# Optimization experiments

Hardware: AMD Instinct MI355X
Metric: run time of the kernel (lower is better)

The kernel has to match this reference:

```python
import jax, jax.numpy as jnp
import numpy as np

B, N = 2, 8192
FUN, EMB = 7, 3
H = 512
HEADS = 8
DH = H // HEADS  # 64
G = 32           # slice_num
L = 4            # n_layers
OUT = 4
MLP_H = 4 * H


def _ln(x, g, b, eps=1e-5):
    m = x.mean(-1, keepdims=True)
    v = ((x - m) ** 2).mean(-1, keepdims=True)
    return (x - m) * jax.lax.rsqrt(v + eps) * g + b


def _forward(fun, emb, W_pre1, b_pre1, W_pre2, b_pre2, placeholder,
             ln1_g, ln1_b, Wfx, bfx, Wx, bx, Wslice, bslice, temp,
             Wq, Wk, Wv, Wo, bo, ln2_g, ln2_b, Wm1, bm1, Wm2, bm2,
             lnf_g, lnf_b, Wout, bout):
    b, n = fun.shape[0], fun.shape[1]
    gelu = lambda z: jax.nn.gelu(z, approximate=False)  # torch nn.GELU default (erf)
    # preprocess MLP (n_layers=0, res=False): act(pre(x)) -> post
    x = jnp.concatenate([emb, fun], axis=-1)            # [B,N,EMB+FUN]
    fx = gelu(x @ W_pre1 + b_pre1) @ W_pre2 + b_pre2    # [B,N,H]
    fx = fx + placeholder
    scale = DH ** -0.5
    for l in range(L):
        # --- physics attention (irregular mesh) ---
        h = _ln(fx, ln1_g[l], ln1_b[l])
        fx_mid = (h @ Wfx[l] + bfx[l]).reshape(b, n, HEADS, DH)  # bnhd
        x_mid = (h @ Wx[l] + bx[l]).reshape(b, n, HEADS, DH)
        logits = jnp.einsum('bnhd,dg->bnhg', x_mid, Wslice[l]) + bslice[l]
        sw = jax.nn.softmax(logits / temp[l][None, None, :, None], axis=-1)  # bnhg
        slice_mass = sw.sum(axis=1)                                   # bhg
        token = jnp.einsum('bnhd,bnhg->bhgd', fx_mid, sw)
        token = token / (slice_mass[..., None] + 1e-5)                # bhgd
        q = token @ Wq[l]
        k = token @ Wk[l]
        v = token @ Wv[l]
        attn = jax.nn.softmax(jnp.einsum('bhgd,bhkd->bhgk', q, k) * scale, axis=-1)
        out_tok = jnp.einsum('bhgk,bhkd->bhgd', attn, v)
        out = jnp.einsum('bhgd,bnhg->bnhd', out_tok, sw).reshape(b, n, H)
        fx = out @ Wo[l] + bo[l] + fx
        # --- LN + MLP (hidden = 4H) with residual ---
        h2 = _ln(fx, ln2_g[l], ln2_b[l])
        fx = gelu(h2 @ Wm1[l] + bm1[l]) @ Wm2[l] + bm2[l] + fx
    # last-layer head: LN -> Linear(out_dim)
    return _ln(fx, lnf_g, lnf_b) @ Wout + bout


def setup_inputs() -> dict:
    key = jax.random.key(0)
    ks = iter(jax.random.split(key, 64))
    nrm = lambda shape, s=0.02: jax.random.normal(next(ks), shape, jnp.float32) * s
    return dict(
        fun=jax.random.normal(next(ks), (B, N, FUN), jnp.float32),
        emb=jax.random.normal(next(ks), (B, N, EMB), jnp.float32),
        W_pre1=nrm((FUN + EMB, 2 * H)), b_pre1=jnp.zeros((2 * H,), jnp.float32),
        W_pre2=nrm((2 * H, H)), b_pre2=jnp.zeros((H,), jnp.float32),
        placeholder=nrm((H,), 1.0),
        ln1_g=jnp.ones((L, H), jnp.float32), ln1_b=jnp.zeros((L, H), jnp.float32),
        Wfx=nrm((L, H, H)), bfx=jnp.zeros((L, H), jnp.float32),
        Wx=nrm((L, H, H)), bx=jnp.zeros((L, H), jnp.float32),
        Wslice=nrm((L, DH, G), 0.1), bslice=jnp.zeros((L, G), jnp.float32),
        temp=jnp.full((L, HEADS), 0.5, jnp.float32),
        Wq=nrm((L, DH, DH)), Wk=nrm((L, DH, DH)), Wv=nrm((L, DH, DH)),
        Wo=nrm((L, H, H)), bo=jnp.zeros((L, H), jnp.float32),
        ln2_g=jnp.ones((L, H), jnp.float32), ln2_b=jnp.zeros((L, H), jnp.float32),
        Wm1=nrm((L, H, MLP_H)), bm1=jnp.zeros((L, MLP_H), jnp.float32),
        Wm2=nrm((L, MLP_H, H)), bm2=jnp.zeros((L, H), jnp.float32),
        lnf_g=jnp.ones((H,), jnp.float32), lnf_b=jnp.zeros((H,), jnp.float32),
        Wout=nrm((H, OUT)), bout=jnp.zeros((OUT,), jnp.float32),
    )


def reference(fun, emb, W_pre1, b_pre1, W_pre2, b_pre2, placeholder,
              ln1_g, ln1_b, Wfx, bfx, Wx, bx, Wslice, bslice, temp,
              Wq, Wk, Wv, Wo, bo, ln2_g, ln2_b, Wm1, bm1, Wm2, bm2,
              lnf_g, lnf_b, Wout, bout):
    return _forward(fun, emb, W_pre1, b_pre1, W_pre2, b_pre2, placeholder,
                    ln1_g, ln1_b, Wfx, bfx, Wx, bx, Wslice, bslice, temp,
                    Wq, Wk, Wv, Wo, bo, ln2_g, ln2_b, Wm1, bm1, Wm2, bm2,
                    lnf_g, lnf_b, Wout, bout)
```

## Files before the change

### kernel.cpp

```cpp
#include <hip/hip_runtime.h>
#include <hip/hip_bf16.h>
#include <cstdint>
#include <cstddef>

typedef float  f32x4  __attribute__((ext_vector_type(4)));
typedef __bf16 bf16x8 __attribute__((ext_vector_type(8)));

#define DEV __device__ __forceinline__

DEV float gelu_f(float x){ return 0.5f * x * (1.0f + erff(x * 0.70710678118654752f)); }

DEV void gl16(void* lds, const void* g){
  __builtin_amdgcn_global_load_lds((const __attribute__((address_space(1))) void*)g,
                                   (__attribute__((address_space(3))) void*)lds, 16, 0, 0);
}

static constexpr size_t OFF_FX     = 0;
static constexpr size_t OFF_H      = 33554432;
static constexpr size_t OFF_REGA   = 50331648;
static constexpr size_t OFF_COMB   = OFF_REGA;
static constexpr size_t OFF_SW     = OFF_REGA + 50331648;
static constexpr size_t OFF_MLPH   = OFF_REGA;
static constexpr size_t OFF_H1     = OFF_REGA;
static constexpr size_t OFF_OUTB   = OFF_REGA + 67108864;
static constexpr size_t OFF_PT     = OFF_OUTB + 16777216;
static constexpr size_t OFF_PTM    = OFF_PT + 2097152;
static constexpr size_t OFF_OT     = OFF_PTM + 32768;
static constexpr size_t OFF_WT     = OFF_OT + 131072;
static constexpr size_t OFF_BIAS   = OFF_WT + 23068672;

__global__ __launch_bounds__(256) void wtrans_k(const float* __restrict__ W, __bf16* __restrict__ Wt,
                                                int K, int N, size_t wstride, size_t wtstride)
{
  __shared__ float tile[64][65];
  W  += (size_t)blockIdx.z * wstride;
  Wt += (size_t)blockIdx.z * wtstride;
  int t = threadIdx.x;
  int k0 = blockIdx.x * 64, n0 = blockIdx.y * 64;
  #pragma unroll
  for (int i = 0; i < 16; i++){
    int e = t + 256*i; int kk = e >> 6, nn = e & 63;
    tile[kk][nn] = W[(size_t)(k0+kk)*N + n0+nn];
  }
  __syncthreads();
  #pragma unroll
  for (int i = 0; i < 16; i++){
    int e = t + 256*i; int nn = e >> 6, kk = e & 63;
    Wt[(size_t)(n0+nn)*K + k0+kk] = (__bf16)tile[kk][nn];
  }
}

__global__ __launch_bounds__(128) void prep_wxs_k(const float* __restrict__ Wx, const float* __restrict__ Wsl,
                                                  const float* __restrict__ bx, const float* __restrict__ bsl,
                                                  const float* __restrict__ temp,
                                                  __bf16* __restrict__ Btcat, float* __restrict__ bcat)
{
  __shared__ float wsc[64];
  int l = blockIdx.y;
  const float* Wx_l  = Wx  + (size_t)l*262144;
  const float* Wsl_l = Wsl + l*2048;
  const float* bx_l  = bx  + l*512;
  const float* bsl_l = bsl + l*32;
  __bf16* Wt_l = Btcat + (size_t)l*393216 + (size_t)512*512;
  float* blog_l = bcat + l*768 + 512;
  int hg = blockIdx.x; int h = hg >> 5, g = hg & 31;
  int t = threadIdx.x;
  if (t < 64) wsc[t] = Wsl_l[t*32 + g];
  __syncthreads();
  float invt = 1.0f / temp[l*8 + h];
  #pragma unroll
  for (int cc = 0; cc < 4; cc++){
    int c = t + cc*128;
    float a = 0.f;
    for (int d = 0; d < 64; d++) a += Wx_l[(size_t)c*512 + h*64 + d] * wsc[d];
    Wt_l[(size_t)hg*512 + c] = (__bf16)(a * invt);
  }
  if (t == 0){
    float a = 0.f;
    for (int d = 0; d < 64; d++) a += bx_l[h*64 + d] * wsc[d];
    blog_l[hg] = (a + bsl_l[g]) * invt;
  }
}

__global__ __launch_bounds__(256) void bias_setup_k(const float* __restrict__ b_pre2, const float* __restrict__ placeholder,
                                                    const float* __restrict__ bfx,
                                                    float* __restrict__ bpre2p, float* __restrict__ bcat)
{
  int i = blockIdx.x*256 + threadIdx.x;
  if (i < 512) bpre2p[i] = b_pre2[i] + placeholder[i];
  else if (i < 2560){
    int j = i - 512; int l = j >> 9, c = j & 511;
    bcat[l*768 + c] = bfx[l*512 + c];
  }
}

__global__ __launch_bounds__(256) void preproc1_k(const float* __restrict__ fun, const float* __restrict__ emb,
                                                  const float* __restrict__ W1, const float* __restrict__ b1,
                                                  __bf16* __restrict__ h1)
{
  __shared__ float w1l[10][1024];
  int t = threadIdx.x;
  for (int i = t*4; i < 10240; i += 1024) *(f32x4*)&w1l[0][i] = *(const f32x4*)&W1[i];
  __syncthreads();
  f32x4 bv = *(const f32x4*)&b1[t*4];
  int r0 = blockIdx.x * 4;
  for (int r = 0; r < 4; r++){
    int m = r0 + r;
    const float* er = emb + (size_t)m*3;
    const float* fr = fun + (size_t)m*7;
    float x[10];
    x[0]=er[0]; x[1]=er[1]; x[2]=er[2];
    #pragma unroll
    for (int c = 0; c < 7; c++) x[3+c] = fr[c];
    f32x4 acc = bv;
    #pragma unroll
    for (int c = 0; c < 10; c++){
      f32x4 wv = *(const f32x4*)&w1l[c][t*4];
      acc += x[c] * wv;
    }
    __bf16* op = h1 + (size_t)m*1024 + t*4;
    #pragma unroll
    for (int e = 0; e < 4; e++) op[e] = (__bf16)gelu_f(acc[e]);
  }
}

template<int EPI, int BN>
__global__ __launch_bounds__(512) void gemm_wide(const __bf16* __restrict__ A, const __bf16* __restrict__ Bt,
                                                 const float* __restrict__ bias, const float* __restrict__ res,
                                                 void* __restrict__ outp, int N, int lgK)
{
  constexpr int NSUB_B = BN/16;
  constexpr int S = 16 + NSUB_B;
  constexpr int Q = S/8;
  constexpr int NJ = BN/32;
  __shared__ bf16x8 ldsAB[3][S][64];
  const int tid = threadIdx.x;
  const int w = tid >> 6, lane = tid & 63;
  const int lm = lane & 15, lq = lane >> 4;
  const int wr = w >> 1, wc = w & 1;
  const int m0 = blockIdx.x * 256, n0 = blockIdx.y * BN;
  const int niter = 1 << (lgK - 5);

  auto issue = [&](int i){
    unsigned buf = (unsigned)i % 3u;
    int kk = i << 5;
    #pragma unroll
    for (int q = 0; q < Q; q++){
      int f = w*Q + q;
      const __bf16* p = (f < 16)
        ? A  + (((size_t)(m0 + f*16 + lm)) << lgK) + kk + lq*8
        : Bt + (((size_t)(n0 + (f-16)*16 + lm)) << lgK) + kk + lq*8;
      gl16(&ldsAB[buf][f][0], p);
    }
  };

  issue(0); issue(1);

  f32x4 acc[4][NJ] = {};

  for (int i = 0; i < niter; ++i){
    if (i + 2 < niter){
      issue(i + 2);
      if constexpr (Q == 4) __builtin_amdgcn_s_waitcnt(0x0F78);
      else                  __builtin_amdgcn_s_waitcnt(0x0F76);
    } else if (i + 1 < niter){
      if constexpr (Q == 4) __builtin_amdgcn_s_waitcnt(0x0F74);
      else                  __builtin_amdgcn_s_waitcnt(0x0F73);
    } else {
      __builtin_amdgcn_s_waitcnt(0x0F70);
    }
    __builtin_amdgcn_s_barrier();
    const unsigned buf = (unsigned)i % 3u;
    bf16x8 af[4], bfr[NJ];
    #pragma unroll
    for (int ii = 0; ii < 4; ii++)  af[ii]  = ldsAB[buf][wr*4 + ii][lane];
    #pragma unroll
    for (int jj = 0; jj < NJ; jj++) bfr[jj] = ldsAB[buf][16 + wc*NJ + jj][lane];
    #pragma unroll
    for (int ii = 0; ii < 4; ii++)
      #pragma unroll
      for (int jj = 0; jj < NJ; jj++)
        acc[ii][jj] = __builtin_amdgcn_mfma_f32_16x16x32_bf16(af[ii], bfr[jj], acc[ii][jj], 0, 0, 0);
    __builtin_amdgcn_s_barrier();
  }

  #pragma unroll
  for (int ii = 0; ii < 4; ii++){
    int row0 = m0 + wr*64 + ii*16 + lq*4;
    #pragma unroll
    for (int jj = 0; jj < NJ; jj++){
      int col = n0 + wc*(BN/2) + jj*16 + lm;
      float bv = bias[col];
      #pragma unroll
      for (int r = 0; r < 4; r++){
        size_t idx = (size_t)(row0 + r)*N + col;
        float v = acc[ii][jj][r] + bv;
        if (EPI == 2) v += res[idx];
        if (EPI == 1) ((__bf16*)outp)[idx] = (__bf16)gelu_f(v);
        else          ((float*)outp)[idx]  = v;
      }
    }
  }
}

__global__ __launch_bounds__(256) void ln_k(const float* __restrict__ x, const float* __restrict__ g,
                                            const float* __restrict__ b, __bf16* __restrict__ out)
{
  int w = threadIdx.x >> 6, lane = threadIdx.x & 63;
  int row = blockIdx.x*4 + w;
  const float* xr = x + (size_t)row*512 + lane*8;
  float v[8];
  *(f32x4*)&v[0] = *(const f32x4*)xr;
  *(f32x4*)&v[4] = *(const f32x4*)(xr + 4);
  float s = 0.f, sq = 0.f;
  #pragma unroll
  for (int e = 0; e < 8; e++){ s += v[e]; sq += v[e]*v[e]; }
  #pragma unroll
  for (int off = 32; off; off >>= 1){ s += __shfl_xor(s, off); sq += __shfl_xor(sq, off); }
  float mean = s * (1.f/512.f);
  float var  = sq * (1.f/512.f) - mean*mean;
  float rstd = rsqrtf(var + 1e-5f);
  float gv[8], bv[8];
  *(f32x4*)&gv[0] = *(const f32x4*)(g + lane*8);
  *(f32x4*)&gv[4] = *(const f32x4*)(g + lane*8 + 4);
  *(f32x4*)&bv[0] = *(const f32x4*)(b + lane*8);
  *(f32x4*)&bv[4] = *(const f32x4*)(b + lane*8 + 4);
  __bf16* op = out + (size_t)row*512 + lane*8;
  #pragma unroll
  for (int e = 0; e < 8; e++) op[e] = (__bf16)((v[e]-mean)*rstd*gv[e] + bv[e]);
}

__global__ __launch_bounds__(256) void softmax_k(const float* __restrict__ comb, float* __restrict__ sw)
{
  int gid = blockIdx.x*256 + threadIdx.x;
  int m = gid >> 3, h = gid & 7;
  const float* lp = comb + (size_t)m*768 + 512 + h*32;
  float x[32];
  #pragma unroll
  for (int i = 0; i < 8; i++) *(f32x4*)&x[i*4] = *(const f32x4*)(lp + i*4);
  float mx = x[0];
  #pragma unroll
  for (int i = 1; i < 32; i++) mx = fmaxf(mx, x[i]);
  float s = 0.f;
  #pragma unroll
  for (int i = 0; i < 32; i++){ x[i] = expf(x[i]-mx); s += x[i]; }
  float inv = 1.f / s;
  int b = m >> 13, n = m & 8191;
  float* op = sw + ((size_t)(b*8 + h)*8192 + n)*32;
  #pragma unroll
  for (int i = 0; i < 8; i++){
    f32x4 t = *(f32x4*)&x[i*4];
    t *= inv;
    *(f32x4*)(op + i*4) = t;
  }
}

__global__ __launch_bounds__(256) void token_part_k(const float* __restrict__ comb, const float* __restrict__ sw,
                                                    float* __restrict__ pt, float* __restrict__ ptm)
{
  __shared__ float fxl[32][64];
  __shared__ float swl[32][32];
  int t = threadIdx.x;
  int chunk = blockIdx.x, bh = blockIdx.y;
  int b = bh >> 3, h = bh & 7;
  int d = t & 63, gg = (t >> 6) * 8;
  float acc[8] = {0,0,0,0,0,0,0,0};
  float macc = 0.f;
  for (int s = 0; s < 16; s++){
    int nbase = chunk*512 + s*32;
    __syncthreads();
    #pragma unroll
    for (int i = 0; i < 2; i++){
      int e = t + 256*i; int rv = e >> 4, c4 = e & 15;
      *(f32x4*)&fxl[rv][c4*4] = *(const f32x4*)&comb[((size_t)b*8192 + nbase + rv)*768 + h*64 + c4*4];
    }
    { int rv = t >> 3, c4 = t & 7;
      *(f32x4*)&swl[rv][c4*4] = *(const f32x4*)&sw[((size_t)bh*8192 + nbase + rv)*32 + c4*4]; }
    __syncthreads();
    for (int nn = 0; nn < 32; nn++){
      float f = fxl[nn][d];
      #pragma unroll
      for (int jj = 0; jj < 8; jj++) acc[jj] += f * swl[nn][gg+jj];
    }
    if (t < 32){ for (int nn = 0; nn < 32; nn++) macc += swl[nn][t]; }
  }
  int cb = chunk*16 + bh;
  #pragma unroll
  for (int jj = 0; jj < 8; jj++)
    pt[((size_t)cb*32 + gg + jj)*64 + d] = acc[jj];
  if (t < 32) ptm[cb*32 + t] = macc;
}

__global__ __launch_bounds__(256) void attn_k(const float* __restrict__ pt, const float* __restrict__ ptm,
                                              const float* __restrict__ Wq, const float* __restrict__ Wk,
                                              const float* __restrict__ Wv, float* __restrict__ ot)
{
  __shared__ float tok[32][64];
  __shared__ float ml[32];
  __shared__ float qq[32][65], kk2[32][65], vv[32][65];
  __shared__ float at[32][33];
  int t = threadIdx.x, bh = blockIdx.x;
  if (t < 32){
    float s = 0.f;
    for (int c = 0; c < 16; c++) s += ptm[(c*16 + bh)*32 + t];
    ml[t] = s + 1e-5f;
  }
  __syncthreads();
  #pragma unroll
  for (int i = 0; i < 8; i++){
    int e = t + 256*i; int g = e >> 6, d = e & 63;
    float s = 0.f;
    for (int c = 0; c < 16; c++) s += pt[((size_t)(c*16 + bh)*32 + g)*64 + d];
    tok[g][d] = s / ml[g];
  }
  __syncthreads();
  #pragma unroll
  for (int i = 0; i < 8; i++){
    int e = t + 256*i; int g = e >> 6, j = e & 63;
    float aq = 0.f, ak = 0.f, av = 0.f;
    for (int d = 0; d < 64; d++){
      float tv = tok[g][d];
      aq += tv * Wq[d*64 + j];
      ak += tv * Wk[d*64 + j];
      av += tv * Wv[d*64 + j];
    }
    qq[g][j] = aq; kk2[g][j] = ak; vv[g][j] = av;
  }
  __syncthreads();
  #pragma unroll
  for (int i = 0; i < 4; i++){
    int e = t + 256*i; int g = e >> 5, j2 = e & 31;
    float s2 = 0.f;
    for (int d = 0; d < 64; d++) s2 += qq[g][d] * kk2[j2][d];
    at[g][j2] = s2 * 0.125f;
  }
  __syncthreads();
  if (t < 32){
    float mx = at[t][0];
    for (int j = 1; j < 32; j++) mx = fmaxf(mx, at[t][j]);
    float ss = 0.f;
    for (int j = 0; j < 32; j++){ float e2 = expf(at[t][j]-mx); at[t][j] = e2; ss += e2; }
    float inv = 1.f / ss;
    for (int j = 0; j < 32; j++) at[t][j] *= inv;
  }
  __syncthreads();
  #pragma unroll
  for (int i = 0; i < 8; i++){
    int e = t + 256*i; int g = e >> 6, d = e & 63;
    float s3 = 0.f;
    for (int j = 0; j < 32; j++) s3 += at[g][j] * vv[j][d];
    ot[(size_t)bh*2048 + e] = s3;
  }
}

__global__ __launch_bounds__(256) void deslice_k(const float* __restrict__ ot, const float* __restrict__ sw,
                                                 __bf16* __restrict__ outb)
{
  __shared__ float otl[32][64];
  __shared__ float swl[4][33];
  int t = threadIdx.x;
  int chunk = blockIdx.x, bh = blockIdx.y;
  int b = bh >> 3, h = bh & 7;
  #pragma unroll
  for (int i = 0; i < 8; i++){
    int e = t + 256*i;
    otl[e>>6][e&63] = ot[(size_t)bh*2048 + e];
  }
  int n0 = chunk*128;
  int nsub = t >> 6, d = t & 63;
  for (int s = 0; s < 32; s++){
    __syncthreads();
    if (t < 128) swl[t>>5][t&31] = sw[((size_t)bh*8192 + n0 + s*4 + (t>>5))*32 + (t&31)];
    __syncthreads();
    float a2 = 0.f;
    #pragma unroll
    for (int g = 0; g < 32; g++) a2 += otl[g][d] * swl[nsub][g];
    int n = n0 + s*4 + nsub;
    outb[((size_t)(b*8192 + n))*512 + h*64 + d] = (__bf16)a2;
  }
}

__global__ __launch_bounds__(256) void head_k(const float* __restrict__ x, const float* __restrict__ g,
                                              const float* __restrict__ b, const float* __restrict__ Wout,
                                              const float* __restrict__ bout, float* __restrict__ out)
{
  int w = threadIdx.x >> 6, lane = threadIdx.x & 63;
  int row = blockIdx.x*4 + w;
  const float* xr = x + (size_t)row*512 + lane*8;
  float v[8];
  *(f32x4*)&v[0] = *(const f32x4*)xr;
  *(f32x4*)&v[4] = *(const f32x4*)(xr + 4);
  float s = 0.f, sq = 0.f;
  #pragma unroll
  for (int e = 0; e < 8; e++){ s += v[e]; sq += v[e]*v[e]; }
  #pragma unroll
  for (int off = 32; off; off >>= 1){ s += __shfl_xor(s, off); sq += __shfl_xor(sq, off); }
  float mean = s * (1.f/512.f);
  float rstd = rsqrtf(sq * (1.f/512.f) - mean*mean + 1e-5f);
  float o[4] = {0,0,0,0};
  #pragma unroll
  for (int e = 0; e < 8; e++){
    int c = lane*8 + e;
    float yn = (v[e]-mean)*rstd*g[c] + b[c];
    const float* wr = Wout + (size_t)c*4;
    o[0] += yn*wr[0]; o[1] += yn*wr[1]; o[2] += yn*wr[2]; o[3] += yn*wr[3];
  }
  #pragma unroll
  for (int off = 32; off; off >>= 1){
    #pragma unroll
    for (int j = 0; j < 4; j++) o[j] += __shfl_xor(o[j], off);
  }
  if (lane == 0){
    #pragma unroll
    for (int j = 0; j < 4; j++) out[(size_t)row*4 + j] = o[j] + bout[j];
  }
}

extern "C" void kernel_launch(void* const* d_in, const int* in_sizes, int n_in,
                              void* d_out, int out_size, void* d_ws, size_t ws_size,
                              hipStream_t stream)
{
  const float* fun    = (const float*)d_in[0];
  const float* emb    = (const float*)d_in[1];
  const float* W_pre1 = (const float*)d_in[2];
  const float* b_pre1 = (const float*)d_in[3];
  const float* W_pre2 = (const float*)d_in[4];
  const float* b_pre2 = (const float*)d_in[5];
  const float* placeholder = (const float*)d_in[6];
  const float* ln1_g  = (const float*)d_in[7];
  const float* ln1_b  = (const float*)d_in[8];
  const float* Wfx    = (const float*)d_in[9];
  const float* bfx    = (const float*)d_in[10];
  const float* Wx     = (const float*)d_in[11];
  const float* bx     = (const float*)d_in[12];
  const float* Wslice = (const float*)d_in[13];
  const float* bslice = (const float*)d_in[14];
  const float* temp   = (const float*)d_in[15];
  const float* Wq     = (const float*)d_in[16];
  const float* Wk     = (const float*)d_in[17];
  const float* Wv     = (const float*)d_in[18];
  const float* Wo     = (const float*)d_in[19];
  const float* bo     = (const float*)d_in[20];
  const float* ln2_g  = (const float*)d_in[21];
  const float* ln2_b  = (const float*)d_in[22];
  const float* Wm1    = (const float*)d_in[23];
  const float* bm1    = (const float*)d_in[24];
  const float* Wm2    = (const float*)d_in[25];
  const float* bm2    = (const float*)d_in[26];
  const float* lnf_g  = (const float*)d_in[27];
  const float* lnf_b  = (const float*)d_in[28];
  const float* Wout   = (const float*)d_in[29];
  const float* bout   = (const float*)d_in[30];

  char* ws = (char*)d_ws;
  float*  fx     = (float*)(ws + OFF_FX);
  __bf16* hbf    = (__bf16*)(ws + OFF_H);
  float*  comb   = (float*)(ws + OFF_COMB);
  float*  sw     = (float*)(ws + OFF_SW);
  __bf16* mlph   = (__bf16*)(ws + OFF_MLPH);
  __bf16* h1bf   = (__bf16*)(ws + OFF_H1);
  __bf16* outb   = (__bf16*)(ws + OFF_OUTB);
  float*  pt     = (float*)(ws + OFF_PT);
  float*  ptm    = (float*)(ws + OFF_PTM);
  float*  ot     = (float*)(ws + OFF_OT);
  __bf16* Wpre2t = (__bf16*)(ws + OFF_WT);
  __bf16* Btcat  = (__bf16*)(ws + OFF_WT + 1048576);
  __bf16* Wot    = (__bf16*)(ws + OFF_WT + 4194304);
  __bf16* Wm1t   = (__bf16*)(ws + OFF_WT + 6291456);
  __bf16* Wm2t   = (__bf16*)(ws + OFF_WT + 14680064);
  float*  bcat   = (float*)(ws + OFF_BIAS);
  float*  bpre2p = (float*)(ws + OFF_BIAS + 4*768*4);

  wtrans_k<<<dim3(16,8,1), 256,0,stream>>>(W_pre2, Wpre2t, 1024, 512, 0, 0);
  wtrans_k<<<dim3(8,8,4),  256,0,stream>>>(Wfx, Btcat, 512, 512, 262144, 393216);
  wtrans_k<<<dim3(8,8,4),  256,0,stream>>>(Wo,  Wot,  512, 512, 262144, 262144);
  wtrans_k<<<dim3(8,32,4), 256,0,stream>>>(Wm1, Wm1t, 512, 2048, 1048576, 1048576);
  wtrans_k<<<dim3(32,8,4), 256,0,stream>>>(Wm2, Wm2t, 2048, 512, 1048576, 1048576);
  prep_wxs_k<<<dim3(256,4),128,0,stream>>>(Wx, Wslice, bx, bslice, temp, Btcat, bcat);
  bias_setup_k<<<10,256,0,stream>>>(b_pre2, placeholder, bfx, bpre2p, bcat);

  preproc1_k<<<4096,256,0,stream>>>(fun, emb, W_pre1, b_pre1, h1bf);
  gemm_wide<0,128><<<dim3(64,4),512,0,stream>>>(h1bf, Wpre2t, bpre2p, nullptr, (void*)fx, 512, 10);

  for (int l = 0; l < 4; l++){
    ln_k<<<4096,256,0,stream>>>(fx, ln1_g + l*512, ln1_b + l*512, hbf);
    gemm_wide<0,256><<<dim3(64,3),512,0,stream>>>(hbf, Btcat + (size_t)l*393216, bcat + l*768, nullptr, (void*)comb, 768, 9);
    softmax_k<<<512,256,0,stream>>>(comb, sw);
    token_part_k<<<dim3(16,16),256,0,stream>>>(comb, sw, pt, ptm);
    attn_k<<<16,256,0,stream>>>(pt, ptm, Wq + l*4096, Wk + l*4096, Wv + l*4096, ot);
    deslice_k<<<dim3(64,16),256,0,stream>>>(ot, sw, outb);
    gemm_wide<2,128><<<dim3(64,4),512,0,stream>>>(outb, Wot + (size_t)l*262144, bo + l*512, fx, (void*)fx, 512, 9);
    ln_k<<<4096,256,0,stream>>>(fx, ln2_g + l*512, ln2_b + l*512, hbf);
    gemm_wide<1,256><<<dim3(64,8),512,0,stream>>>(hbf, Wm1t + (size_t)l*1048576, bm1 + l*2048, nullptr, (void*)mlph, 2048, 9);
    gemm_wide<2,128><<<dim3(64,4),512,0,stream>>>(mlph, Wm2t + (size_t)l*1048576, bm2 + l*512, fx, (void*)fx, 512, 11);
  }

  head_k<<<4096,256,0,stream>>>(fx, lnf_g, lnf_b, Wout, bout, (float*)d_out);
}
```

Before: 1.439 ms.

## Fuse slice softmax into projection GEMM epilogue and use double-buffered LDS

The per-head slice softmax moves into the epilogue of the combined fx/x/slice-logit GEMM. Blocks covering the logit columns compute the softmax with 16-lane shuffles and write slice weights directly, so the separate softmax kernel and its reread of the logits are gone. The GEMM pipeline also drops from triple to double LDS buffering with a prefetch distance of one. That reduces shared memory use, which may raise occupancy, but exposes more global-load latency. The epilogue writes are scalar strided stores rather than vectorized ones.

```diff
diff --git a/kernel.cpp b/kernel.cpp
--- a/kernel.cpp
+++ b/kernel.cpp
@@ -127,13 +127,14 @@
 template<int EPI, int BN>
 __global__ __launch_bounds__(512) void gemm_wide(const __bf16* __restrict__ A, const __bf16* __restrict__ Bt,
                                                  const float* __restrict__ bias, const float* __restrict__ res,
-                                                 void* __restrict__ outp, int N, int lgK)
+                                                 void* __restrict__ outp, void* __restrict__ outp2,
+                                                 int N, int lgK)
 {
   constexpr int NSUB_B = BN/16;
   constexpr int S = 16 + NSUB_B;
   constexpr int Q = S/8;
   constexpr int NJ = BN/32;
-  __shared__ bf16x8 ldsAB[3][S][64];
+  __shared__ bf16x8 ldsAB[2][S][64];
   const int tid = threadIdx.x;
   const int w = tid >> 6, lane = tid & 63;
   const int lm = lane & 15, lq = lane >> 4;
@@ -142,7 +143,7 @@
   const int niter = 1 << (lgK - 5);
 
   auto issue = [&](int i){
-    unsigned buf = (unsigned)i % 3u;
+    unsigned buf = (unsigned)i & 1u;
     int kk = i << 5;
     #pragma unroll
     for (int q = 0; q < Q; q++){
@@ -154,23 +155,20 @@
     }
   };
 
-  issue(0); issue(1);
+  issue(0);
 
   f32x4 acc[4][NJ] = {};
 
   for (int i = 0; i < niter; ++i){
-    if (i + 2 < niter){
-      issue(i + 2);
-      if constexpr (Q == 4) __builtin_amdgcn_s_waitcnt(0x0F78);
-      else                  __builtin_amdgcn_s_waitcnt(0x0F76);
-    } else if (i + 1 < niter){
+    if (i + 1 < niter){
+      issue(i + 1);
       if constexpr (Q == 4) __builtin_amdgcn_s_waitcnt(0x0F74);
       else                  __builtin_amdgcn_s_waitcnt(0x0F73);
     } else {
       __builtin_amdgcn_s_waitcnt(0x0F70);
     }
     __builtin_amdgcn_s_barrier();
-    const unsigned buf = (unsigned)i % 3u;
+    const unsigned buf = (unsigned)i & 1u;
     bf16x8 af[4], bfr[NJ];
     #pragma unroll
     for (int ii = 0; ii < 4; ii++)  af[ii]  = ldsAB[buf][wr*4 + ii][lane];
@@ -182,6 +180,40 @@
       for (int jj = 0; jj < NJ; jj++)
         acc[ii][jj] = __builtin_amdgcn_mfma_f32_16x16x32_bf16(af[ii], bfr[jj], acc[ii][jj], 0, 0, 0);
     __builtin_amdgcn_s_barrier();
+  }
+
+  if (EPI == 4 && blockIdx.y == 2){
+    float* swp = (float*)outp2;
+    #pragma unroll
+    for (int ii = 0; ii < 4; ii++){
+      int row0 = m0 + wr*64 + ii*16 + lq*4;
+      #pragma unroll
+      for (int hp = 0; hp < 4; hp++){
+        int j0 = hp*2, j1 = j0 + 1;
+        int h = wc*4 + hp;
+        float b0 = bias[512 + wc*128 + j0*16 + lm];
+        float b1 = bias[512 + wc*128 + j1*16 + lm];
+        #pragma unroll
+        for (int r = 0; r < 4; r++){
+          int row = row0 + r;
+          float v0 = acc[ii][j0][r] + b0;
+          float v1 = acc[ii][j1][r] + b1;
+          float mx = fmaxf(v0, v1);
+          #pragma unroll
+          for (int msk = 8; msk; msk >>= 1) mx = fmaxf(mx, __shfl_xor(mx, msk));
+          float e0 = expf(v0 - mx), e1 = expf(v1 - mx);
+          float ss = e0 + e1;
+          #pragma unroll
+          for (int msk = 8; msk; msk >>= 1) ss += __shfl_xor(ss, msk);
+          float inv = 1.f / ss;
+          int b = row >> 13, n = row & 8191;
+          float* op = swp + ((size_t)(b*8 + h)*8192 + n)*32;
+          op[lm]      = e0 * inv;
+          op[16 + lm] = e1 * inv;
+        }
+      }
+    }
+    return;
   }
 
   #pragma unroll
@@ -228,31 +260,6 @@
   __bf16* op = out + (size_t)row*512 + lane*8;
   #pragma unroll
   for (int e = 0; e < 8; e++) op[e] = (__bf16)((v[e]-mean)*rstd*gv[e] + bv[e]);
-}
-
-__global__ __launch_bounds__(256) void softmax_k(const float* __restrict__ comb, float* __restrict__ sw)
-{
-  int gid = blockIdx.x*256 + threadIdx.x;
-  int m = gid >> 3, h = gid & 7;
-  const float* lp = comb + (size_t)m*768 + 512 + h*32;
-  float x[32];
-  #pragma unroll
-  for (int i = 0; i < 8; i++) *(f32x4*)&x[i*4] = *(const f32x4*)(lp + i*4);
-  float mx = x[0];
-  #pragma unroll
-  for (int i = 1; i < 32; i++) mx = fmaxf(mx, x[i]);
-  float s = 0.f;
-  #pragma unroll
-  for (int i = 0; i < 32; i++){ x[i] = expf(x[i]-mx); s += x[i]; }
-  float inv = 1.f / s;
-  int b = m >> 13, n = m & 8191;
-  float* op = sw + ((size_t)(b*8 + h)*8192 + n)*32;
-  #pragma unroll
-  for (int i = 0; i < 8; i++){
-    f32x4 t = *(f32x4*)&x[i*4];
-    t *= inv;
-    *(f32x4*)(op + i*4) = t;
-  }
 }
 
 __global__ __launch_bounds__(256) void token_part_k(const float* __restrict__ comb, const float* __restrict__ sw,
@@ -480,19 +487,18 @@
   bias_setup_k<<<10,256,0,stream>>>(b_pre2, placeholder, bfx, bpre2p, bcat);
 
   preproc1_k<<<4096,256,0,stream>>>(fun, emb, W_pre1, b_pre1, h1bf);
-  gemm_wide<0,128><<<dim3(64,4),512,0,stream>>>(h1bf, Wpre2t, bpre2p, nullptr, (void*)fx, 512, 10);
+  gemm_wide<0,128><<<dim3(64,4),512,0,stream>>>(h1bf, Wpre2t, bpre2p, nullptr, (void*)fx, nullptr, 512, 10);
 
   for (int l = 0; l < 4; l++){
     ln_k<<<4096,256,0,stream>>>(fx, ln1_g + l*512, ln1_b + l*512, hbf);
-    gemm_wide<0,256><<<dim3(64,3),512,0,stream>>>(hbf, Btcat + (size_t)l*393216, bcat + l*768, nullptr, (void*)comb, 768, 9);
-    softmax_k<<<512,256,0,stream>>>(comb, sw);
+    gemm_wide<4,256><<<dim3(64,3),512,0,stream>>>(hbf, Btcat + (size_t)l*393216, bcat + l*768, nullptr, (void*)comb, (void*)sw, 768, 9);
     token_part_k<<<dim3(16,16),256,0,stream>>>(comb, sw, pt, ptm);
     attn_k<<<16,256,0,stream>>>(pt, ptm, Wq + l*4096, Wk + l*4096, Wv + l*4096, ot);
     deslice_k<<<dim3(64,16),256,0,stream>>>(ot, sw, outb);
-    gemm_wide<2,128><<<dim3(64,4),512,0,stream>>>(outb, Wot + (size_t)l*262144, bo + l*512, fx, (void*)fx, 512, 9);
+    gemm_wide<2,128><<<dim3(64,4),512,0,stream>>>(outb, Wot + (size_t)l*262144, bo + l*512, fx, (void*)fx, nullptr, 512, 9);
     ln_k<<<4096,256,0,stream>>>(fx, ln2_g + l*512, ln2_b + l*512, hbf);
-    gemm_wide<1,256><<<dim3(64,8),512,0,stream>>>(hbf, Wm1t + (size_t)l*1048576, bm1 + l*2048, nullptr, (void*)mlph, 2048, 9);
-    gemm_wide<2,128><<<dim3(64,4),512,0,stream>>>(mlph, Wm2t + (size_t)l*1048576, bm2 + l*512, fx, (void*)fx, 512, 11);
+    gemm_wide<1,256><<<dim3(64,8),512,0,stream>>>(hbf, Wm1t + (size_t)l*1048576, bm1 + l*2048, nullptr, (void*)mlph, nullptr, 2048, 9);
+    gemm_wide<2,128><<<dim3(64,4),512,0,stream>>>(mlph, Wm2t + (size_t)l*1048576, bm2 + l*512, fx, (void*)fx, nullptr, 512, 11);
   }
 
   head_k<<<4096,256,0,stream>>>(fx, lnf_g, lnf_b, Wout, bout, (float*)d_out);
```

Result: slower. 1.927 ms (+33.9%).
